# Optimization experiments

Hardware: AMD Instinct MI355X
Metric: run time of the kernel (lower is better)

The kernel has to match this reference:

```python
import jax, jax.numpy as jnp
import numpy as np

Y0 = 0.28209479177387814  # Y_0^0 spherical harmonic (degree-0 basis)
CUTOFF = 4.6
K_COUL = 0.529
ENERGY_STD = 1.0
HEADS = 8
N, E, C, L, MID = 32768, 524288, 16, 4, 32
KC = C // 2  # channels_div = 2 -> key/value channels


def _radial(ef, W1, b1, W2, b2, W3, b3):
    # radial profile MLP producing per-edge conv weights
    h = jax.nn.relu(ef @ W1 + b1)
    h = jax.nn.relu(h @ W2 + b2)
    return h @ W3 + b3


def _conv_msg(x_src, ef, bscale, W1, b1, W2, b2, W3, b3, c_out, c_in):
    # degree-0 tensor-field conv: per-edge weight matrix times source feats, times basis
    R = _radial(ef, W1, b1, W2, b2, W3, b3).reshape(-1, c_out, c_in)
    return jnp.einsum('eoi,ei->eo', R, x_src) * bscale[:, None]


def _forward(species, src, dst, rel_pos, emb, kv_W1, kv_b1, kv_W2, kv_b2, kv_W3, kv_b3, Wq, Wproj, fin_W1, fin_b1, fin_W2, fin_b2, fin_W3, fin_b3, Wself, mlp_W1, mlp_b1, mlp_W2, mlp_b2, mlp_W3, mlp_b3):
    n = species.shape[0]
    dist = jnp.linalg.norm(rel_pos, axis=1)
    xc = dist / CUTOFF
    in_cut = dist < CUTOFF
    x2 = jnp.minimum(jnp.where(in_cut, xc * xc, 0.0), 1.0 - 1e-6)
    scale = jnp.where(in_cut, jnp.exp(3.0 - 3.0 / (1.0 - x2)), 0.0)  # bump_fn k=3
    bscale = Y0 * scale  # basis scaled by cutoff envelope per edge
    semb = emb[species - 1]          # [N,C]
    x = semb                         # degree-0 node feats
    # edge feats: (C-1) zero radial-basis channels + distance
    ef = jnp.concatenate([jnp.zeros((dist.shape[0], C - 1), dist.dtype), dist[:, None]], axis=1)
    dh = KC // HEADS
    for l in range(kv_W1.shape[0]):
        kv = _conv_msg(x[src], ef, bscale, kv_W1[l], kv_b1[l], kv_W2[l], kv_b2[l], kv_W3[l], kv_b3[l], 2 * KC, C)
        val, key_ = kv[:, :KC], kv[:, KC:]
        q = x @ Wq[l].T              # [N,KC]
        logits = jnp.einsum('ehd,ehd->eh', key_.reshape(-1, HEADS, dh), q[dst].reshape(-1, HEADS, dh)) / np.sqrt(dh)
        mx = jax.ops.segment_max(logits, dst, num_segments=n)
        w = scale[:, None] * jnp.exp(logits - mx[dst])   # weighted edge softmax
        denom = jax.ops.segment_sum(w, dst, num_segments=n)
        attn = w / jnp.maximum(denom[dst], 1e-20)
        z = (attn[:, :, None] * val.reshape(-1, HEADS, dh)).reshape(-1, KC)
        agg = jax.ops.segment_sum(z, dst, num_segments=n)
        x = jnp.concatenate([agg, x], axis=1) @ Wproj[l].T  # project(cat(attn_out, skip))
        ef = ef + x[src]             # edge feature update via copy_u
    m = _conv_msg(x[src], ef, bscale, fin_W1, fin_b1, fin_W2, fin_b2, fin_W3, fin_b3, C, C)
    feats = jax.ops.segment_sum(m, dst, num_segments=n) + x @ Wself.T  # pooled conv + self-interaction
    cat = jnp.concatenate([semb, feats], axis=1)
    h = jax.nn.silu(cat @ mlp_W1 + mlp_b1)
    h = jax.nn.silu(h @ mlp_W2 + mlp_b2)
    learned = (h @ mlp_W3 + mlp_b3)[:, 0]
    Z = species.astype(dist.dtype)
    Zu, Zv = Z[src], Z[dst]
    raw = K_COUL * Zu * Zv / (2.0 * dist)
    au = 0.8854 * 0.529 / (Zu ** 0.23 + Zv ** 0.23)
    xx = dist / au
    screen = (0.1818 * jnp.exp(-3.2 * xx) + 0.5099 * jnp.exp(-0.9423 * xx)
              + 0.2802 * jnp.exp(-0.4028 * xx) + 0.02817 * jnp.exp(-0.2016 * xx))
    coul = jax.ops.segment_sum(raw * screen * scale, dst, num_segments=n) / ENERGY_STD
    atom_e = (learned + coul) * ENERGY_STD
    return jnp.sum(atom_e)  # SumPooling over a single graph, forces=False


def setup_inputs() -> dict:
    key = jax.random.key(0)
    ks = jax.random.split(key, 32)
    species = jax.random.randint(ks[0], (N,), 1, 90, dtype=jnp.int32)
    src = jax.random.randint(ks[1], (E,), 0, N, dtype=jnp.int32)
    dst = jax.random.randint(ks[2], (E,), 0, N, dtype=jnp.int32)
    d = jax.random.normal(ks[3], (E, 3))
    d = d / jnp.linalg.norm(d, axis=1, keepdims=True)
    r = jax.random.uniform(ks[4], (E, 1), minval=0.5, maxval=5.5)
    rel_pos = (d * r).astype(jnp.float32)
    g = lambda k, sh, fan: (jax.random.normal(k, sh) / np.sqrt(fan)).astype(jnp.float32)
    return dict(
        species=species, src=src, dst=dst, rel_pos=rel_pos,
        emb=g(ks[5], (100, C), 1),
        kv_W1=g(ks[6], (L, C, MID), C), kv_b1=jnp.zeros((L, MID), jnp.float32),
        kv_W2=g(ks[7], (L, MID, MID), MID), kv_b2=jnp.zeros((L, MID), jnp.float32),
        kv_W3=g(ks[8], (L, MID, 2 * KC * C), MID), kv_b3=jnp.zeros((L, 2 * KC * C), jnp.float32),
        Wq=g(ks[9], (L, KC, C), C),
        Wproj=g(ks[10], (L, C, KC + C), KC + C),
        fin_W1=g(ks[11], (C, MID), C), fin_b1=jnp.zeros((MID,), jnp.float32),
        fin_W2=g(ks[12], (MID, MID), MID), fin_b2=jnp.zeros((MID,), jnp.float32),
        fin_W3=g(ks[13], (MID, C * C), MID), fin_b3=jnp.zeros((C * C,), jnp.float32),
        Wself=g(ks[14], (C, C), C),
        mlp_W1=g(ks[15], (2 * C, C), 2 * C), mlp_b1=jnp.zeros((C,), jnp.float32),
        mlp_W2=g(ks[16], (C, C), C), mlp_b2=jnp.zeros((C,), jnp.float32),
        mlp_W3=g(ks[17], (C, 1), C), mlp_b3=jnp.zeros((1,), jnp.float32),
    )


def reference(species, src, dst, rel_pos, emb, kv_W1, kv_b1, kv_W2, kv_b2, kv_W3, kv_b3, Wq, Wproj, fin_W1, fin_b1, fin_W2, fin_b2, fin_W3, fin_b3, Wself, mlp_W1, mlp_b1, mlp_W2, mlp_b2, mlp_W3, mlp_b3):
    return _forward(species, src, dst, rel_pos, emb, kv_W1, kv_b1, kv_W2, kv_b2, kv_W3, kv_b3, Wq, Wproj, fin_W1, fin_b1, fin_W2, fin_b2, fin_W3, fin_b3, Wself, mlp_W1, mlp_b1, mlp_W2, mlp_b2, mlp_W3, mlp_b3)
```

## Files before the change

### kernel.cpp

```cpp
#include <hip/hip_runtime.h>

constexpr float F_Y0     = 0.28209479177387814f;
constexpr float F_CUTOFF = 4.6f;

typedef short short8 __attribute__((ext_vector_type(8)));
typedef float f32x4  __attribute__((ext_vector_type(4)));
typedef float float2v __attribute__((ext_vector_type(2)));

__device__ __forceinline__ float siluf(float v) { return v / (1.0f + __expf(-v)); }

__device__ __forceinline__ unsigned pk2(float a, float b) {
  unsigned r;
  asm("v_cvt_pk_bf16_f32 %0, %1, %2" : "=v"(r) : "v"(a), "v"(b));
  return r;
}
__device__ __forceinline__ float xbf(unsigned d, int h) {
  return __uint_as_float(h ? (d & 0xffff0000u) : (d << 16));
}
__device__ __forceinline__ float2v pkmul2(float2v a, float2v b) {
  float2v d;
  asm("v_pk_mul_f32 %0, %1, %2" : "=v"(d) : "v"(a), "v"(b));
  return d;
}

union FragU { uint4 u; short8 s; };

__device__ __forceinline__ void load16(const float* p, float* r) {
  const float4* p4 = (const float4*)p;
#pragma unroll
  for (int i = 0; i < 4; i++) {
    float4 t = p4[i];
    r[4*i] = t.x; r[4*i+1] = t.y; r[4*i+2] = t.z; r[4*i+3] = t.w;
  }
}
__device__ __forceinline__ void store16(float* p, const float* r) {
  float4* p4 = (float4*)p;
#pragma unroll
  for (int i = 0; i < 4; i++) p4[i] = make_float4(r[4*i], r[4*i+1], r[4*i+2], r[4*i+3]);
}

__device__ __forceinline__ void block_reduce_store(float v, float* part) {
  __shared__ float sred[4];
  int tid = threadIdx.x;
#pragma unroll
  for (int off = 32; off > 0; off >>= 1) v += __shfl_down(v, off, 64);
  if ((tid & 63) == 0) sred[tid >> 6] = v;
  __syncthreads();
  if (tid == 0) part[blockIdx.x] = sred[0] + sred[1] + sred[2] + sred[3];
}

__global__ __launch_bounds__(256) void k_pre(
    const int* __restrict__ species, const int* __restrict__ src, const int* __restrict__ dst,
    const float* __restrict__ rel_pos,
    float* __restrict__ dist_, float* __restrict__ scale_,
    int* __restrict__ cnt,
    float* __restrict__ coul_part, int E)
{
  __shared__ float zpow[128];
  int tid = threadIdx.x;
  if (tid < 128) zpow[tid] = __powf((float)tid, 0.23f);
  __syncthreads();

  int e = blockIdx.x * 256 + tid;
  float ce = 0.0f;
  if (e < E) {
    float px = rel_pos[3*(size_t)e + 0];
    float py = rel_pos[3*(size_t)e + 1];
    float pz = rel_pos[3*(size_t)e + 2];
    float dist = sqrtf(px*px + py*py + pz*pz);
    float xc = dist * (1.0f / F_CUTOFF);
    bool in_cut = dist < F_CUTOFF;
    float x2 = in_cut ? xc * xc : 0.0f;
    x2 = fminf(x2, 1.0f - 1e-6f);
    float sc = in_cut ? __expf(3.0f - 3.0f / (1.0f - x2)) : 0.0f;
    dist_[e] = dist;
    scale_[e] = sc;
    atomicAdd(&cnt[dst[e]], 1);
    int spu = species[src[e]], spv = species[dst[e]];
    float Zu = (float)spu;
    float Zv = (float)spv;
    float raw = 0.529f * Zu * Zv / (2.0f * dist);
    float au = 0.8854f * 0.529f / (zpow[spu] + zpow[spv]);
    float xx = dist / au;
    float screen = 0.1818f   * __expf(-3.2f    * xx)
                 + 0.5099f   * __expf(-0.9423f * xx)
                 + 0.2802f   * __expf(-0.4028f * xx)
                 + 0.02817f  * __expf(-0.2016f * xx);
    ce = raw * screen * sc;
  }
  block_reduce_store(ce, coul_part);
}

__global__ __launch_bounds__(256) void k_scan1(
    const int* __restrict__ cnt, int* __restrict__ row_ptr, int* __restrict__ bsum)
{
  __shared__ int s[256];
  int tid = threadIdx.x;
  int n = blockIdx.x * 256 + tid;
  int v = cnt[n];
  s[tid] = v;
  __syncthreads();
#pragma unroll
  for (int off = 1; off < 256; off <<= 1) {
    int t = (tid >= off) ? s[tid - off] : 0;
    __syncthreads();
    s[tid] += t;
    __syncthreads();
  }
  row_ptr[n] = s[tid] - v;
  if (tid == 255) bsum[blockIdx.x] = s[255];
}

__global__ __launch_bounds__(128) void k_scan2(int* __restrict__ bsum, int* __restrict__ boff)
{
  __shared__ int s[128];
  int tid = threadIdx.x;
  int v = bsum[tid];
  s[tid] = v;
  __syncthreads();
#pragma unroll
  for (int off = 1; off < 128; off <<= 1) {
    int t = (tid >= off) ? s[tid - off] : 0;
    __syncthreads();
    s[tid] += t;
    __syncthreads();
  }
  boff[tid] = s[tid] - v;
}

__global__ __launch_bounds__(256) void k_scan3(
    int* __restrict__ row_ptr, int* __restrict__ row_cur,
    const int* __restrict__ boff, int N, int E)
{
  int n = blockIdx.x * 256 + threadIdx.x;
  int rp = row_ptr[n] + boff[blockIdx.x];
  row_ptr[n] = rp;
  row_cur[n] = rp;
  if (n == 0) row_ptr[N] = E;
}

__global__ __launch_bounds__(256) void k_scatter_perm(
    const int* __restrict__ dst, int* __restrict__ row_cur,
    int* __restrict__ perm, int E)
{
  int e = blockIdx.x * 256 + threadIdx.x;
  if (e >= E) return;
  int pos = atomicAdd(&row_cur[dst[e]], 1);
  perm[pos] = e;
}

__global__ __launch_bounds__(256) void k_permute(
    const int* __restrict__ perm,
    const int* __restrict__ src, const float* __restrict__ dist_, const float* __restrict__ scale_,
    int* __restrict__ srcP, float* __restrict__ distP, float* __restrict__ scaleP, int E)
{
  int i = blockIdx.x * 256 + threadIdx.x;
  if (i >= E) return;
  int e = perm[i];
  srcP[i]   = src[e];
  distP[i]  = dist_[e];
  scaleP[i] = scale_[e];
}

__global__ __launch_bounds__(256) void k_prepack(
    const float* __restrict__ kv_W3, const float* __restrict__ kv_b3,
    const float* __restrict__ fin_W3, const float* __restrict__ fin_b3,
    const float* __restrict__ kv_W2, const float* __restrict__ fin_W2,
    const float* __restrict__ kv_W1, const float* __restrict__ fin_W1,
    uint4* __restrict__ WF)
{
  int t = blockIdx.x * 256 + threadIdx.x;
  if (t >= 5 * 21 * 64) return;
  int lyr = t / (21 * 64);
  int rem = t - lyr * 21 * 64;
  int f = rem >> 6;
  int l = rem & 63;
  int qq = l >> 4;
  int o = l & 15;
  const float* W3 = (lyr < 4) ? (kv_W3 + (size_t)lyr * 32 * 256) : fin_W3;
  const float* B3 = (lyr < 4) ? (kv_b3 + (size_t)lyr * 256) : fin_b3;
  const float* W2 = (lyr < 4) ? (kv_W2 + (size_t)lyr * 32 * 32) : fin_W2;
  const float* W1 = (lyr < 4) ? (kv_W1 + (size_t)lyr * 16 * 32) : fin_W1;
  float v[8];
#pragma unroll
  for (int j = 0; j < 8; j++) {
    if (f < 16) {
      int kk = f * 32 + qq * 8 + j;
      int m = kk >> 4, i = kk & 15;
      v[j] = W3[m * 256 + o * 16 + i];
    } else if (f == 16) {
      int r = qq * 8 + j;
      int mp = r >> 4, i = r & 15;
      v[j] = mp ? 0.0f : B3[o * 16 + i];
    } else if (f < 19) {
      int c = f - 17;
      int p = qq * 8 + j;
      int m = (p & 1) ? (16 + (p >> 1)) : (p >> 1);
      v[j] = W2[m * 32 + c * 16 + o];
    } else {
      int c = f - 19;
      int k = qq * 8 + j;
      v[j] = (k < 16) ? W1[k * 32 + c * 16 + o] : 0.0f;
    }
  }
  uint4 dw;
  dw.x = pk2(v[0], v[1]);
  dw.y = pk2(v[2], v[3]);
  dw.z = pk2(v[4], v[5]);
  dw.w = pk2(v[6], v[7]);
  WF[t] = dw;
}

__global__ __launch_bounds__(256) void k_node_init(
    const int* __restrict__ species, const float* __restrict__ emb,
    const float* __restrict__ Wq0,
    float* __restrict__ x, float* __restrict__ q, int N)
{
  int n = blockIdx.x * 256 + threadIdx.x;
  if (n >= N) return;
  int sp = species[n] - 1;
  float xv[16];
  load16(emb + (size_t)sp * 16, xv);
  store16(x + (size_t)n * 16, xv);
  float qv[8];
#pragma unroll
  for (int h = 0; h < 8; h++) {
    float a = 0.f;
#pragma unroll
    for (int i = 0; i < 16; i++) a += Wq0[h * 16 + i] * xv[i];
    qv[h] = a;
  }
  float4* qp = (float4*)(q + (size_t)n * 8);
  qp[0] = make_float4(qv[0], qv[1], qv[2], qv[3]);
  qp[1] = make_float4(qv[4], qv[5], qv[6], qv[7]);
}

template <int MODE>
__global__ __launch_bounds__(256, 7) void k_edge_conv(
    const int* __restrict__ srcP,
    const float* __restrict__ scaleP, const float* __restrict__ distP,
    const float* __restrict__ xsum, const float* __restrict__ x,
    const float* __restrict__ W1, const float* __restrict__ B1,
    const float* __restrict__ B2,
    const uint4* __restrict__ WF,
    unsigned* __restrict__ kvB, int E)
{
  __shared__ unsigned smem[4 * 1344];
  int tid = threadIdx.x;
  int w = __builtin_amdgcn_readfirstlane(tid >> 6);
  int l = tid & 63;
  int quad = l >> 4;
  int lo = l & 15;
  unsigned* WS  = smem + w * 1344;
  unsigned* P   = WS;
  float*    xsS = (float*)WS;
  unsigned* xsB = WS + 320;
  unsigned* efB = WS + 512;
  unsigned* h1P = WS + 704;
  unsigned* h2P = WS + 1024;

  int ebw = blockIdx.x * 64 + w * 16;

  float b2a = B2[lo], b2b = B2[16 + lo];
  float scv[4];
#pragma unroll
  for (int r = 0; r < 4; r++) scv[r] = scaleP[ebw + quad * 4 + r];

  {
    int e4 = l >> 2, c4 = l & 3;
    int s4 = srcP[ebw + e4];
    float4 xv4 = ((const float4*)(x + (size_t)s4 * 16))[c4];
    float4 ev4;
    if (MODE == 2) {
      ev4 = ((const float4*)(xsum + (size_t)s4 * 16))[c4];
      if (c4 == 3) ev4.w += distP[ebw + e4];
    }
    *(float4*)&xsS[e4 * 20 + c4 * 4] = xv4;
    uint2 xp; xp.x = pk2(xv4.x, xv4.y); xp.y = pk2(xv4.z, xv4.w);
    *(uint2*)&xsB[e4 * 12 + c4 * 2] = xp;
    if (MODE == 2) {
      uint2 ep; ep.x = pk2(ev4.x, ev4.y); ep.y = pk2(ev4.z, ev4.w);
      *(uint2*)&efB[e4 * 12 + c4 * 2] = ep;
    }
  }

  if (MODE == 0) {
    float dd = distP[ebw + lo];
#pragma unroll
    for (int jj = 0; jj < 4; jj++) {
      int d = quad * 4 + jj;
      float v0 = fmaxf(B1[d]      + dd * W1[15 * 32 + d],      0.f);
      float v1 = fmaxf(B1[d + 16] + dd * W1[15 * 32 + d + 16], 0.f);
      h1P[lo * 20 + d] = pk2(v0, v1);
    }
  } else {
    float b1a = B1[lo], b1b = B1[16 + lo];
    FragU a, b0, b1;
    uint4 r = *(const uint4*)&efB[lo * 12 + (quad & 1) * 4];
    uint4 z = make_uint4(0, 0, 0, 0);
    a.u = (quad >= 2) ? z : r;
    b0.u = WF[19 * 64 + l];
    b1.u = WF[20 * 64 + l];
    f32x4 c0 = {0.f, 0.f, 0.f, 0.f};
    f32x4 c1 = {0.f, 0.f, 0.f, 0.f};
    c0 = __builtin_amdgcn_mfma_f32_16x16x32_bf16(a.s, b0.s, c0, 0, 0, 0);
    c1 = __builtin_amdgcn_mfma_f32_16x16x32_bf16(a.s, b1.s, c1, 0, 0, 0);
#pragma unroll
    for (int r2 = 0; r2 < 4; r2++)
      h1P[(quad * 4 + r2) * 20 + lo] =
          pk2(fmaxf(c0[r2] + b1a, 0.f), fmaxf(c1[r2] + b1b, 0.f));
  }

  {
    FragU a, b0, b1;
    a.u = *(const uint4*)&h1P[lo * 20 + quad * 4];
    b0.u = WF[17 * 64 + l];
    b1.u = WF[18 * 64 + l];
    f32x4 hc0 = {0.f, 0.f, 0.f, 0.f};
    f32x4 hc1 = {0.f, 0.f, 0.f, 0.f};
    hc0 = __builtin_amdgcn_mfma_f32_16x16x32_bf16(a.s, b0.s, hc0, 0, 0, 0);
    hc1 = __builtin_amdgcn_mfma_f32_16x16x32_bf16(a.s, b1.s, hc1, 0, 0, 0);
#pragma unroll
    for (int r = 0; r < 4; r++)
      h2P[(quad * 4 + r) * 20 + lo] =
          pk2(fmaxf(hc0[r] + b2a, 0.f), fmaxf(hc1[r] + b2b, 0.f));
  }

  float2v xs2[8];
  {
    const float4* xr = (const float4*)&xsS[lo * 20];
#pragma unroll
    for (int i = 0; i < 4; i++) {
      float4 t = xr[i];
      float2v a; a.x = t.x; a.y = t.y;
      float2v b; b.x = t.z; b.y = t.w;
      xs2[2 * i]     = a;
      xs2[2 * i + 1] = b;
    }
  }
  uint2 hA = *(const uint2*)&h2P[lo * 20 + quad * 2];
  uint2 hB = *(const uint2*)&h2P[lo * 20 + 8 + quad * 2];
  float hmv[8];
  hmv[0] = xbf(hA.x, 0); hmv[1] = xbf(hA.y, 0);
  hmv[2] = xbf(hB.x, 0); hmv[3] = xbf(hB.y, 0);
  hmv[4] = xbf(hA.x, 1); hmv[5] = xbf(hA.y, 1);
  hmv[6] = xbf(hB.x, 1); hmv[7] = xbf(hB.y, 1);

  f32x4 acc = {0.f, 0.f, 0.f, 0.f};
  {
    FragU a, b;
    uint4 r = *(const uint4*)&xsB[lo * 12 + (quad & 1) * 4];
    uint4 z = make_uint4(0, 0, 0, 0);
    a.u = (quad >= 2) ? z : r;
    b.u = WF[16 * 64 + l];
    acc = __builtin_amdgcn_mfma_f32_16x16x32_bf16(a.s, b.s, acc, 0, 0, 0);
  }

#pragma unroll
  for (int q = 0; q < 4; q++) {
#pragma unroll
    for (int j = 0; j < 2; j++) {
      float hm = hmv[q * 2 + j];
      float2v hm2; hm2.x = hm; hm2.y = hm;
      uint4 d0, d1;
      float2v p0 = pkmul2(hm2, xs2[0]);
      float2v p1 = pkmul2(hm2, xs2[1]);
      float2v p2 = pkmul2(hm2, xs2[2]);
      float2v p3 = pkmul2(hm2, xs2[3]);
      d0.x = pk2(p0.x, p0.y); d0.y = pk2(p1.x, p1.y);
      d0.z = pk2(p2.x, p2.y); d0.w = pk2(p3.x, p3.y);
      float2v p4 = pkmul2(hm2, xs2[4]);
      float2v p5 = pkmul2(hm2, xs2[5]);
      float2v p6 = pkmul2(hm2, xs2[6]);
      float2v p7 = pkmul2(hm2, xs2[7]);
      d1.x = pk2(p4.x, p4.y); d1.y = pk2(p5.x, p5.y);
      d1.z = pk2(p6.x, p6.y); d1.w = pk2(p7.x, p7.y);
      int cb = quad * 4 + j * 2;
      *(uint4*)&P[lo * 64 + (((cb)     ^ lo) << 2)] = d0;
      *(uint4*)&P[lo * 64 + (((cb + 1) ^ lo) << 2)] = d1;
    }
#pragma unroll
    for (int t = 0; t < 4; t++) {
      FragU a, b;
      a.u = *(const uint4*)&P[lo * 64 + (((t * 4 + quad) ^ lo) << 2)];
      b.u = WF[(q * 4 + t) * 64 + l];
      acc = __builtin_amdgcn_mfma_f32_16x16x32_bf16(a.s, b.s, acc, 0, 0, 0);
    }
  }

#pragma unroll
  for (int r = 0; r < 4; r++) {
    int e = quad * 4 + r;
    ((float*)h2P)[e * 20 + lo] = acc[r] * (F_Y0 * scv[r]);
  }
  {
    int e2 = l >> 2, c = l & 3;
    const float* row = (const float*)&h2P[e2 * 20 + c * 4];
    float4 t = *(const float4*)row;
    uint2 pkd;
    pkd.x = pk2(t.x, t.y);
    pkd.y = pk2(t.z, t.w);
    *(uint2*)(kvB + ((size_t)(ebw + e2) * 8 + c * 2)) = pkd;
  }
}

template <bool INIT>
__global__ __launch_bounds__(256) void k_agg_update(
    const int* __restrict__ row_ptr, const float* __restrict__ scaleP,
    const unsigned* __restrict__ kvB, const float* __restrict__ qin,
    const float* __restrict__ xin,
    const float* __restrict__ Wproj, const float* __restrict__ Wq_next,
    float* __restrict__ xout, float* __restrict__ qout, float* __restrict__ xsum, int N)
{
  __shared__ float sA[16 * 8];
  __shared__ float sX[16 * 17];
  __shared__ float sN[16 * 17];
  int tid = threadIdx.x;
  int nl = tid >> 4;
  int t16 = tid & 15;
  int h = t16 & 7;
  int p = t16 >> 3;
  int n = blockIdx.x * 16 + nl;
  int hd = h >> 1, hh = h & 1;

  float qh = qin[(size_t)n * 8 + h];
  int j0 = row_ptr[n], j1 = row_ptr[n + 1];
  float num = 0.f, den = 0.f;
  int j = j0 + p;
  for (; j + 6 < j1; j += 8) {
    unsigned va = kvB[(size_t)j * 8 + hd];
    unsigned ka = kvB[(size_t)j * 8 + 4 + hd];
    unsigned vb = kvB[(size_t)(j + 2) * 8 + hd];
    unsigned kb = kvB[(size_t)(j + 2) * 8 + 4 + hd];
    unsigned vc = kvB[(size_t)(j + 4) * 8 + hd];
    unsigned kc = kvB[(size_t)(j + 4) * 8 + 4 + hd];
    unsigned vd = kvB[(size_t)(j + 6) * 8 + hd];
    unsigned kd = kvB[(size_t)(j + 6) * 8 + 4 + hd];
    float sa = scaleP[j];
    float sb = scaleP[j + 2];
    float sc = scaleP[j + 4];
    float sd = scaleP[j + 6];
    float wa = sa * __expf(fminf(xbf(ka, hh) * qh, 60.0f));
    float wb = sb * __expf(fminf(xbf(kb, hh) * qh, 60.0f));
    float wc = sc * __expf(fminf(xbf(kc, hh) * qh, 60.0f));
    float wd = sd * __expf(fminf(xbf(kd, hh) * qh, 60.0f));
    num += wa * xbf(va, hh) + wb * xbf(vb, hh) + wc * xbf(vc, hh) + wd * xbf(vd, hh);
    den += (wa + wb) + (wc + wd);
  }
  for (; j < j1; j += 2) {
    float val = xbf(kvB[(size_t)j * 8 + hd], hh);
    float key = xbf(kvB[(size_t)j * 8 + 4 + hd], hh);
    float lg = fminf(key * qh, 60.0f);
    float wv = scaleP[j] * __expf(lg);
    num += wv * val;
    den += wv;
  }
  num += __shfl_xor(num, 8, 64);
  den += __shfl_xor(den, 8, 64);
  if (p == 0) sA[nl * 8 + h] = num / fmaxf(den, 1e-20f);
  sX[nl * 17 + t16] = xin[(size_t)n * 16 + t16];
  __syncthreads();

  float cat[24];
#pragma unroll
  for (int jj = 0; jj < 8; jj++) cat[jj] = sA[nl * 8 + jj];
#pragma unroll
  for (int jj = 0; jj < 16; jj++) cat[8 + jj] = sX[nl * 17 + jj];
  float xn = 0.f;
#pragma unroll
  for (int jj = 0; jj < 24; jj++) xn += Wproj[t16 * 24 + jj] * cat[jj];
  xout[(size_t)n * 16 + t16] = xn;
  if (INIT) {
    xsum[(size_t)n * 16 + t16] = xn;
  } else {
    xsum[(size_t)n * 16 + t16] += xn;
  }
  sN[nl * 17 + t16] = xn;
  __syncthreads();

  if (p == 0) {
    float a = 0.f;
#pragma unroll
    for (int i = 0; i < 16; i++) a += Wq_next[h * 16 + i] * sN[nl * 17 + i];
    qout[(size_t)n * 8 + h] = a;
  }
}

__global__ __launch_bounds__(256) void k_feats_final(
    const int* __restrict__ row_ptr, const unsigned* __restrict__ kvB,
    const float* __restrict__ x,
    const int* __restrict__ species, const float* __restrict__ emb,
    const float* __restrict__ Wself,
    const float* __restrict__ mW1, const float* __restrict__ mb1,
    const float* __restrict__ mW2, const float* __restrict__ mb2,
    const float* __restrict__ mW3, const float* __restrict__ mb3,
    float* __restrict__ learn_part, int N)
{
  __shared__ float sX[16 * 20];
  __shared__ float sC[16 * 40];
  __shared__ float sH[16 * 20];
  int tid = threadIdx.x;
  int nl = tid >> 4;
  int o = tid & 15;
  int n = blockIdx.x * 16 + nl;
  int od = o >> 1, oh = o & 1;

  int j0 = row_ptr[n], j1 = row_ptr[n + 1];
  float ft = 0.f;
  int j = j0;
  for (; j + 3 < j1; j += 4) {
    unsigned a = kvB[(size_t)j * 8 + od];
    unsigned b = kvB[(size_t)(j + 1) * 8 + od];
    unsigned c = kvB[(size_t)(j + 2) * 8 + od];
    unsigned d = kvB[(size_t)(j + 3) * 8 + od];
    ft += (xbf(a, oh) + xbf(b, oh)) + (xbf(c, oh) + xbf(d, oh));
  }
  for (; j < j1; ++j) ft += xbf(kvB[(size_t)j * 8 + od], oh);

  if (o < 4) {
    float4 v = ((const float4*)(x + (size_t)n * 16))[o];
    *(float4*)&sX[nl * 20 + o * 4] = v;
  } else if (o < 8) {
    int sp = species[n] - 1;
    float4 v = ((const float4*)(emb + (size_t)sp * 16))[o - 4];
    *(float4*)&sC[nl * 40 + (o - 4) * 4] = v;
  }
  __syncthreads();

  float xv[16];
  load16(&sX[nl * 20], xv);
  float a = ft;
#pragma unroll
  for (int i = 0; i < 16; i++) a += Wself[o * 16 + i] * xv[i];
  sC[nl * 40 + 16 + o] = a;
  __syncthreads();

  float cat[32];
  load16(&sC[nl * 40], cat);
  load16(&sC[nl * 40 + 16], cat + 16);
  float hh = mb1[o];
#pragma unroll
  for (int k = 0; k < 32; k++) hh += cat[k] * mW1[k * 16 + o];
  hh = siluf(hh);
  sH[nl * 20 + o] = hh;
  __syncthreads();

  float hv[16];
  load16(&sH[nl * 20], hv);
  float h2 = mb2[o];
#pragma unroll
  for (int k = 0; k < 16; k++) h2 += hv[k] * mW2[k * 16 + o];
  h2 = siluf(h2);
  float contrib = h2 * mW3[o] + ((o == 0) ? mb3[0] : 0.f);
  block_reduce_store(contrib, learn_part);
}

__global__ __launch_bounds__(256) void k_finalize(
    const float* __restrict__ coul_part, int nc,
    const float* __restrict__ learn_part, int nl,
    float* __restrict__ out)
{
  __shared__ float sred[4];
  int tid = threadIdx.x;
  float v = 0.f;
  for (int i = tid; i < nc; i += 256) v += coul_part[i];
  for (int i = tid; i < nl; i += 256) v += learn_part[i];
#pragma unroll
  for (int off = 32; off > 0; off >>= 1) v += __shfl_down(v, off, 64);
  if ((tid & 63) == 0) sred[tid >> 6] = v;
  __syncthreads();
  if (tid == 0) out[0] = sred[0] + sred[1] + sred[2] + sred[3];
}

extern "C" void kernel_launch(void* const* d_in, const int* in_sizes, int n_in,
                              void* d_out, int out_size, void* d_ws, size_t ws_size,
                              hipStream_t stream)
{
  const int*   species = (const int*)d_in[0];
  const int*   src     = (const int*)d_in[1];
  const int*   dst     = (const int*)d_in[2];
  const float* rel_pos = (const float*)d_in[3];
  const float* emb     = (const float*)d_in[4];
  const float* kv_W1   = (const float*)d_in[5];
  const float* kv_b1   = (const float*)d_in[6];
  const float* kv_W2   = (const float*)d_in[7];
  const float* kv_b2   = (const float*)d_in[8];
  const float* kv_W3   = (const float*)d_in[9];
  const float* kv_b3   = (const float*)d_in[10];
  const float* Wq      = (const float*)d_in[11];
  const float* Wproj   = (const float*)d_in[12];
  const float* fin_W1  = (const float*)d_in[13];
  const float* fin_b1  = (const float*)d_in[14];
  const float* fin_W2  = (const float*)d_in[15];
  const float* fin_b2  = (const float*)d_in[16];
  const float* fin_W3  = (const float*)d_in[17];
  const float* fin_b3  = (const float*)d_in[18];
  const float* Wself   = (const float*)d_in[19];
  const float* mlp_W1  = (const float*)d_in[20];
  const float* mlp_b1  = (const float*)d_in[21];
  const float* mlp_W2  = (const float*)d_in[22];
  const float* mlp_b2  = (const float*)d_in[23];
  const float* mlp_W3  = (const float*)d_in[24];
  const float* mlp_b3  = (const float*)d_in[25];

  const int N = in_sizes[0];
  const int E = in_sizes[1];
  const int nblk_e = (E + 255) / 256;
  const int nblk_n = (N + 255) / 256;
  const int nblk_f = N / 16;

  char* p = (char*)d_ws;
  auto alloc = [&](size_t bytes) -> void* {
    void* r = (void*)p;
    p += (bytes + 255) & ~(size_t)255;
    return r;
  };
  float*    dist_   = (float*)alloc((size_t)E * 4);
  float*    scale_  = (float*)alloc((size_t)E * 4);
  float*    distP   = (float*)alloc((size_t)E * 4);
  float*    scaleP  = (float*)alloc((size_t)E * 4);
  int*      srcP    = (int*)  alloc((size_t)E * 4);
  int*      perm    = (int*)  alloc((size_t)E * 4);
  unsigned* kvB     = (unsigned*)alloc((size_t)E * 8 * 4);
  float*    xA      = (float*)alloc((size_t)N * 16 * 4);
  float*    xB      = (float*)alloc((size_t)N * 16 * 4);
  float*    xsum    = (float*)alloc((size_t)N * 16 * 4);
  float*    q       = (float*)alloc((size_t)N * 8 * 4);
  int*      cnt     = (int*)  alloc((size_t)N * 4);
  int*      row_ptr = (int*)  alloc((size_t)(N + 1) * 4);
  int*      row_cur = (int*)  alloc((size_t)N * 4);
  int*      bsum    = (int*)  alloc(128 * 4);
  int*      boff    = (int*)  alloc(128 * 4);
  uint4*    WF      = (uint4*)alloc((size_t)5 * 21 * 64 * 16);
  float*    coul_part  = (float*)alloc((size_t)nblk_e * 4);
  float*    learn_part = (float*)alloc((size_t)nblk_f * 4);

  dim3 blk(256);
  dim3 egrid(nblk_e);
  dim3 cgrid(E / 64);
  dim3 ngrid(nblk_n);
  dim3 augrid(N / 16);
  dim3 fgrid(nblk_f);

  hipMemsetAsync(cnt, 0, (size_t)N * 4, stream);

  k_prepack<<<dim3(27), blk, 0, stream>>>(kv_W3, kv_b3, fin_W3, fin_b3,
                                          kv_W2, fin_W2, kv_W1, fin_W1, WF);

  k_pre<<<egrid, blk, 0, stream>>>(species, src, dst, rel_pos, dist_, scale_,
                                   cnt, coul_part, E);
  k_scan1<<<ngrid, blk, 0, stream>>>(cnt, row_ptr, bsum);
  k_scan2<<<dim3(1), dim3(128), 0, stream>>>(bsum, boff);
  k_scan3<<<ngrid, blk, 0, stream>>>(row_ptr, row_cur, boff, N, E);
  k_scatter_perm<<<egrid, blk, 0, stream>>>(dst, row_cur, perm, E);
  k_permute<<<egrid, blk, 0, stream>>>(perm, src, dist_, scale_,
                                       srcP, distP, scaleP, E);

  k_node_init<<<ngrid, blk, 0, stream>>>(species, emb, Wq, xA, q, N);

  float* xin = xA;
  float* xout = xB;
  for (int l = 0; l < 4; l++) {
    const float* W1 = kv_W1 + (size_t)l * 16 * 32;
    const float* B1 = kv_b1 + (size_t)l * 32;
    const float* B2 = kv_b2 + (size_t)l * 32;
    const uint4* WFl = WF + (size_t)l * 21 * 64;
    const float* Wqn = Wq + (size_t)((l < 3) ? (l + 1) : 0) * 8 * 16;
    if (l == 0) {
      k_edge_conv<0><<<cgrid, blk, 0, stream>>>(srcP, scaleP, distP, xsum, xin,
                                                W1, B1, B2, WFl, kvB, E);
    } else {
      k_edge_conv<2><<<cgrid, blk, 0, stream>>>(srcP, scaleP, distP, xsum, xin,
                                                W1, B1, B2, WFl, kvB, E);
    }
    if (l == 0) {
      k_agg_update<true><<<augrid, blk, 0, stream>>>(row_ptr, scaleP, kvB, q, xin,
                                                     Wproj, Wqn, xout, q, xsum, N);
    } else {
      k_agg_update<false><<<augrid, blk, 0, stream>>>(row_ptr, scaleP, kvB, q, xin,
                                                      Wproj + (size_t)l * 16 * 24, Wqn,
                                                      xout, q, xsum, N);
    }
    float* tmp = xin; xin = xout; xout = tmp;
  }

  k_edge_conv<2><<<cgrid, blk, 0, stream>>>(srcP, scaleP, distP, xsum, xin,
                                            fin_W1, fin_b1, fin_b2,
                                            WF + (size_t)4 * 21 * 64, kvB, E);
  k_feats_final<<<fgrid, blk, 0, stream>>>(row_ptr, kvB, xin, species, emb, Wself,
                                           mlp_W1, mlp_b1, mlp_W2, mlp_b2, mlp_W3, mlp_b3,
                                           learn_part, N);
  k_finalize<<<dim3(1), blk, 0, stream>>>(coul_part, nblk_e, learn_part, nblk_f,
                                          (float*)d_out);
}
```

Before: 408.6 us.

## Compact edge list to in-cutoff edges and skip out-of-cutoff work

Edges with zero cutoff envelope are excluded from the CSR counts, the permutation and the Coulomb term. The active edge count is read on the device from row_ptr[N]. Edge-conv blocks past that count exit early, which cuts radial-MLP and gather work in proportion to the fraction of edges outside the cutoff. Padding entries of srcP, distP and scaleP are prefilled with neutral values so the tail of a partial block stays harmless, at the cost of extra writes in k_pre.

```diff
diff --git a/kernel.cpp b/kernel.cpp
--- a/kernel.cpp
+++ b/kernel.cpp
@@ -54,7 +54,8 @@
     const float* __restrict__ rel_pos,
     float* __restrict__ dist_, float* __restrict__ scale_,
     int* __restrict__ cnt,
-    float* __restrict__ coul_part, int E)
+    float* __restrict__ coul_part,
+    int* __restrict__ srcP, float* __restrict__ distP, float* __restrict__ scaleP, int E)
 {
   __shared__ float zpow[128];
   int tid = threadIdx.x;
@@ -75,18 +76,23 @@
     float sc = in_cut ? __expf(3.0f - 3.0f / (1.0f - x2)) : 0.0f;
     dist_[e] = dist;
     scale_[e] = sc;
-    atomicAdd(&cnt[dst[e]], 1);
-    int spu = species[src[e]], spv = species[dst[e]];
-    float Zu = (float)spu;
-    float Zv = (float)spv;
-    float raw = 0.529f * Zu * Zv / (2.0f * dist);
-    float au = 0.8854f * 0.529f / (zpow[spu] + zpow[spv]);
-    float xx = dist / au;
-    float screen = 0.1818f   * __expf(-3.2f    * xx)
-                 + 0.5099f   * __expf(-0.9423f * xx)
-                 + 0.2802f   * __expf(-0.4028f * xx)
-                 + 0.02817f  * __expf(-0.2016f * xx);
-    ce = raw * screen * sc;
+    srcP[e]   = 0;
+    distP[e]  = 1.0f;
+    scaleP[e] = 0.0f;
+    if (sc > 0.0f) {
+      atomicAdd(&cnt[dst[e]], 1);
+      int spu = species[src[e]], spv = species[dst[e]];
+      float Zu = (float)spu;
+      float Zv = (float)spv;
+      float raw = 0.529f * Zu * Zv / (2.0f * dist);
+      float au = 0.8854f * 0.529f / (zpow[spu] + zpow[spv]);
+      float xx = dist / au;
+      float screen = 0.1818f   * __expf(-3.2f    * xx)
+                   + 0.5099f   * __expf(-0.9423f * xx)
+                   + 0.2802f   * __expf(-0.4028f * xx)
+                   + 0.02817f  * __expf(-0.2016f * xx);
+      ce = raw * screen * sc;
+    }
   }
   block_reduce_store(ce, coul_part);
 }
@@ -130,32 +136,36 @@
 
 __global__ __launch_bounds__(256) void k_scan3(
     int* __restrict__ row_ptr, int* __restrict__ row_cur,
-    const int* __restrict__ boff, int N, int E)
+    const int* __restrict__ boff, const int* __restrict__ cnt, int N)
 {
   int n = blockIdx.x * 256 + threadIdx.x;
   int rp = row_ptr[n] + boff[blockIdx.x];
   row_ptr[n] = rp;
   row_cur[n] = rp;
-  if (n == 0) row_ptr[N] = E;
+  if (n == N - 1) row_ptr[N] = rp + cnt[n];
 }
 
 __global__ __launch_bounds__(256) void k_scatter_perm(
-    const int* __restrict__ dst, int* __restrict__ row_cur,
+    const int* __restrict__ dst, const float* __restrict__ scale_,
+    int* __restrict__ row_cur,
     int* __restrict__ perm, int E)
 {
   int e = blockIdx.x * 256 + threadIdx.x;
   if (e >= E) return;
-  int pos = atomicAdd(&row_cur[dst[e]], 1);
-  perm[pos] = e;
+  if (scale_[e] > 0.0f) {
+    int pos = atomicAdd(&row_cur[dst[e]], 1);
+    perm[pos] = e;
+  }
 }
 
 __global__ __launch_bounds__(256) void k_permute(
     const int* __restrict__ perm,
     const int* __restrict__ src, const float* __restrict__ dist_, const float* __restrict__ scale_,
-    int* __restrict__ srcP, float* __restrict__ distP, float* __restrict__ scaleP, int E)
+    int* __restrict__ srcP, float* __restrict__ distP, float* __restrict__ scaleP,
+    const int* __restrict__ eactp)
 {
   int i = blockIdx.x * 256 + threadIdx.x;
-  if (i >= E) return;
+  if (i >= eactp[0]) return;
   int e = perm[i];
   srcP[i]   = src[e];
   distP[i]  = dist_[e];
@@ -243,8 +253,9 @@
     const float* __restrict__ W1, const float* __restrict__ B1,
     const float* __restrict__ B2,
     const uint4* __restrict__ WF,
-    unsigned* __restrict__ kvB, int E)
-{
+    unsigned* __restrict__ kvB, const int* __restrict__ eactp)
+{
+  if (blockIdx.x * 64 >= eactp[0]) return;
   __shared__ unsigned smem[4 * 1344];
   int tid = threadIdx.x;
   int w = __builtin_amdgcn_readfirstlane(tid >> 6);
@@ -635,6 +646,8 @@
   float*    coul_part  = (float*)alloc((size_t)nblk_e * 4);
   float*    learn_part = (float*)alloc((size_t)nblk_f * 4);
 
+  const int* eactp = row_ptr + N;
+
   dim3 blk(256);
   dim3 egrid(nblk_e);
   dim3 cgrid(E / 64);
@@ -648,13 +661,13 @@
                                           kv_W2, fin_W2, kv_W1, fin_W1, WF);
 
   k_pre<<<egrid, blk, 0, stream>>>(species, src, dst, rel_pos, dist_, scale_,
-                                   cnt, coul_part, E);
+                                   cnt, coul_part, srcP, distP, scaleP, E);
   k_scan1<<<ngrid, blk, 0, stream>>>(cnt, row_ptr, bsum);
   k_scan2<<<dim3(1), dim3(128), 0, stream>>>(bsum, boff);
-  k_scan3<<<ngrid, blk, 0, stream>>>(row_ptr, row_cur, boff, N, E);
-  k_scatter_perm<<<egrid, blk, 0, stream>>>(dst, row_cur, perm, E);
+  k_scan3<<<ngrid, blk, 0, stream>>>(row_ptr, row_cur, boff, cnt, N);
+  k_scatter_perm<<<egrid, blk, 0, stream>>>(dst, scale_, row_cur, perm, E);
   k_permute<<<egrid, blk, 0, stream>>>(perm, src, dist_, scale_,
-                                       srcP, distP, scaleP, E);
+                                       srcP, distP, scaleP, eactp);
 
   k_node_init<<<ngrid, blk, 0, stream>>>(species, emb, Wq, xA, q, N);
 
@@ -668,10 +681,10 @@
     const float* Wqn = Wq + (size_t)((l < 3) ? (l + 1) : 0) * 8 * 16;
     if (l == 0) {
       k_edge_conv<0><<<cgrid, blk, 0, stream>>>(srcP, scaleP, distP, xsum, xin,
-                                                W1, B1, B2, WFl, kvB, E);
+                                                W1, B1, B2, WFl, kvB, eactp);
     } else {
       k_edge_conv<2><<<cgrid, blk, 0, stream>>>(srcP, scaleP, distP, xsum, xin,
-                                                W1, B1, B2, WFl, kvB, E);
+                                                W1, B1, B2, WFl, kvB, eactp);
     }
     if (l == 0) {
       k_agg_update<true><<<augrid, blk, 0, stream>>>(row_ptr, scaleP, kvB, q, xin,
@@ -686,7 +699,7 @@
 
   k_edge_conv<2><<<cgrid, blk, 0, stream>>>(srcP, scaleP, distP, xsum, xin,
                                             fin_W1, fin_b1, fin_b2,
-                                            WF + (size_t)4 * 21 * 64, kvB, E);
+                                            WF + (size_t)4 * 21 * 64, kvB, eactp);
   k_feats_final<<<fgrid, blk, 0, stream>>>(row_ptr, kvB, xin, species, emb, Wself,
                                            mlp_W1, mlp_b1, mlp_W2, mlp_b2, mlp_W3, mlp_b3,
                                            learn_part, N);
```

Result: faster. 369.7 us (-9.5%).
